# Optimization experiments

Measured on AMD Instinct MI355X. Metric: run time of the kernel, lower is better.

The kernel has to match this reference:

```python
import jax, jax.numpy as jnp
import numpy as np

S, T, H, D = 4096, 4096, 16, 64
N_EMBD = H * D

def setup_inputs() -> dict:
    key = jax.random.key(0)
    kq, kk, kv, kw = jax.random.split(key, 4)
    q = jax.random.normal(kq, (S, H, D), dtype=jnp.float32)
    k = jax.random.normal(kk, (T, H, D), dtype=jnp.float32)
    v = jax.random.normal(kv, (T, H, D), dtype=jnp.float32)
    # GPT-2 style init: std = 0.02 / sqrt(2 * n_layer), n_layer = 24
    W_proj = jax.random.normal(kw, (N_EMBD, N_EMBD), dtype=jnp.float32) * (0.02 / np.sqrt(2 * 24))
    return {"q": q, "k": k, "v": v, "W_proj": W_proj}

def reference(q, k, v, W_proj):
    s, h, d = q.shape
    t = k.shape[0]
    # causal bias: mask positions where query index < key index (future keys)
    causal_bias = (jnp.arange(s)[:, None] < jnp.arange(t)[None, :]).astype(jnp.float32) * -10000.0
    scale = 1.0 / jnp.sqrt(jnp.float32(d))
    # [h, s, t] scores in fp32 (matches original .astype(jnp.float32))
    scores = jnp.einsum('shd,thd->hst', q, k).astype(jnp.float32) * scale + causal_bias
    attn = jax.nn.softmax(scores, axis=-1).astype(q.dtype)
    # dropout p=0 / inference -> identity
    out = jnp.einsum('hst,thd->shd', attn, v).reshape(s, h * d)
    # nn.Linear (no bias) vmapped over tokens: y = x @ W.T
    return out @ W_proj.T
```

## Files before the change

kernel.cpp:

```cpp
#include <hip/hip_runtime.h>

#define S_LEN 4096
#define NH 16
#define DH 64
#define NE 1024

typedef __bf16 bf16_t;
typedef __bf16 bf16x8 __attribute__((ext_vector_type(8)));
typedef __bf16 bf16x4 __attribute__((ext_vector_type(4)));
typedef __bf16 bf16x2 __attribute__((ext_vector_type(2)));
typedef float  f32x4  __attribute__((ext_vector_type(4)));

#define QSCALE 0.180336879f

__global__ __launch_bounds__(256) void pack_all(const float* __restrict__ q,
                                                const float* __restrict__ k,
                                                const float* __restrict__ w,
                                                const float* __restrict__ v,
                                                bf16_t* __restrict__ qb,
                                                bf16_t* __restrict__ kb,
                                                bf16_t* __restrict__ wb,
                                                bf16_t* __restrict__ vt) {
    __shared__ bf16_t tile[64][65];
    const int bid = blockIdx.x;
    if (bid < 4096) {
        const int tid = bid * 256 + threadIdx.x;
        const int e = tid * 4;
        const int s = e >> 10;
        const int c = e & (NE - 1);
        const int h = c >> 6;
        const int d = c & (DH - 1);
        const int o = (h * S_LEN + s) * DH + d;
        float4 qv = *(const float4*)(q + e);
        float4 kv = *(const float4*)(k + e);
        bf16x4 qo, ko;
        qo[0] = (bf16_t)(qv.x * QSCALE); qo[1] = (bf16_t)(qv.y * QSCALE);
        qo[2] = (bf16_t)(qv.z * QSCALE); qo[3] = (bf16_t)(qv.w * QSCALE);
        ko[0] = (bf16_t)kv.x; ko[1] = (bf16_t)kv.y; ko[2] = (bf16_t)kv.z; ko[3] = (bf16_t)kv.w;
        *(bf16x4*)(qb + o) = qo;
        *(bf16x4*)(kb + o) = ko;
        if (tid < (NE * NE / 4)) {
            float4 wv = *(const float4*)(w + tid * 4);
            bf16x4 wo;
            wo[0] = (bf16_t)wv.x; wo[1] = (bf16_t)wv.y; wo[2] = (bf16_t)wv.z; wo[3] = (bf16_t)wv.w;
            *(bf16x4*)(wb + tid * 4) = wo;
        }
    } else {
        const int vb = bid - 4096;
        const int h  = vb >> 6;
        const int t0 = (vb & 63) * 64;
        const int r  = threadIdx.x >> 6;
        const int cl = threadIdx.x & 63;
#pragma unroll
        for (int rep = 0; rep < 16; ++rep) {
            int i = rep * 4 + r;
            tile[cl][i] = (bf16_t)v[(t0 + i) * NE + h * DH + cl];
        }
        __syncthreads();
        const int r2  = threadIdx.x >> 5;
        const int cl2 = (threadIdx.x & 31) * 2;
#pragma unroll
        for (int rep = 0; rep < 8; ++rep) {
            int d = rep * 8 + r2;
            bf16x2 out;
            out[0] = tile[d][cl2];
            out[1] = tile[d][cl2 + 1];
            *(bf16x2*)(vt + (h * DH + d) * S_LEN + t0 + cl2) = out;
        }
    }
}

__global__ __launch_bounds__(512, 4) void attn(const bf16_t* __restrict__ qb,
                                               const bf16_t* __restrict__ kb,
                                               const bf16_t* __restrict__ vt,
                                               float* __restrict__ po,
                                               float* __restrict__ ls) {
    __shared__ __align__(16) bf16_t kbuf[2][64 * 72];
    __shared__ __align__(16) bf16_t vbuf[2][64 * 72];
    __shared__ __align__(16) bf16_t pbuf[8][16 * 72];

    const int tid  = threadIdx.x;
    const int wave = tid >> 6;
    const int lane = tid & 63;
    const int l15  = lane & 15;
    const int quad = lane >> 4;
    const int h = blockIdx.x;
    const int x = blockIdx.y;

    const int sA = x;
    const int sB = 31 - x;
    const int n0 = x + 1;
    const int b1 = sB + 1;
    const int N  = 33;

    const bf16_t* __restrict__ qh = qb + h * (S_LEN * DH);
    const bf16_t* __restrict__ kh = kb + h * (S_LEN * DH);
    const bf16_t* __restrict__ vh = vt + h * (DH * S_LEN);

    const int row0 = tid >> 3;
    const int tc8  = (tid & 7) * 8;

    f32x4 o_acc[4];
    float lsum[4];
    bf16x8 qA[2];
    int s0 = sA * 128 + wave * 16;

    auto load_q = [&](int s0_) {
#pragma unroll
        for (int dc = 0; dc < 2; ++dc)
            qA[dc] = *(const bf16x8*)(qh + (s0_ + l15) * DH + dc * 32 + quad * 8);
    };
    auto reset_acc = [&]() {
#pragma unroll
        for (int db = 0; db < 4; ++db) o_acc[db] = (f32x4){0.f, 0.f, 0.f, 0.f};
#pragma unroll
        for (int r = 0; r < 4; ++r) lsum[r] = 0.0f;
    };
    auto epilogue = [&](int s0_, int slot) {
        float l2[4];
#pragma unroll
        for (int r = 0; r < 4; ++r) l2[r] = lsum[r];
#pragma unroll
        for (int off = 8; off >= 1; off >>= 1)
#pragma unroll
            for (int r = 0; r < 4; ++r) l2[r] += __shfl_xor(l2[r], off, 64);
        float* poz = po + (size_t)(slot * NH + h) * S_LEN * DH;
#pragma unroll
        for (int db = 0; db < 4; ++db)
#pragma unroll
            for (int r = 0; r < 4; ++r)
                poz[(s0_ + quad * 4 + r) * DH + db * 16 + l15] = o_acc[db][r];
        if (l15 == 0) {
            float* lsz = ls + (size_t)(slot * NH + h) * S_LEN;
#pragma unroll
            for (int r = 0; r < 4; ++r) lsz[s0_ + quad * 4 + r] = l2[r];
        }
    };

    load_q(s0);
    reset_acc();

    {
        bf16x8 kr = *(const bf16x8*)(kh + row0 * DH + tc8);
        bf16x8 vr = *(const bf16x8*)(vh + row0 * S_LEN + tc8);
        *(bf16x8*)(kbuf[0] + row0 * 72 + tc8) = kr;
        *(bf16x8*)(vbuf[0] + row0 * 72 + tc8) = vr;
    }
    __syncthreads();

    for (int j = 0; j < N; ++j) {
        if (j == n0) {
            epilogue(s0, 0);
            s0 = sB * 128 + wave * 16;
            load_q(s0);
            reset_acc();
        }
        const int t0 = (j < n0 ? j : b1 + (j - n0)) * 64;
        const bf16_t* kb_ = kbuf[j & 1];
        const bf16_t* vb_ = vbuf[j & 1];

        bf16x8 krn, vrn;
        const bool pf = (j + 1 < N);
        if (pf) {
            const int jn = j + 1;
            const int tn = (jn < n0 ? jn : b1 + (jn - n0)) * 64;
            krn = *(const bf16x8*)(kh + (tn + row0) * DH + tc8);
            vrn = *(const bf16x8*)(vh + row0 * S_LEN + tn + tc8);
        }

        f32x4 c_[4];
#pragma unroll
        for (int ch = 0; ch < 4; ++ch) {
            bf16x8 kB0 = *(const bf16x8*)(kb_ + (ch * 16 + l15) * 72 + quad * 8);
            bf16x8 kB1 = *(const bf16x8*)(kb_ + (ch * 16 + l15) * 72 + 32 + quad * 8);
            f32x4 zr = (f32x4){0.f, 0.f, 0.f, 0.f};
            zr = __builtin_amdgcn_mfma_f32_16x16x32_bf16(qA[0], kB0, zr, 0, 0, 0);
            zr = __builtin_amdgcn_mfma_f32_16x16x32_bf16(qA[1], kB1, zr, 0, 0, 0);
            c_[ch] = zr;
        }

        if (t0 + 63 > s0) {
#pragma unroll
            for (int ch = 0; ch < 4; ++ch) {
                int col = t0 + ch * 16 + l15;
#pragma unroll
                for (int r = 0; r < 4; ++r) {
                    int row = s0 + quad * 4 + r;
                    if (col > row) c_[ch][r] = -INFINITY;
                }
            }
        }

        bf16_t* pl = pbuf[wave];
#pragma unroll
        for (int ch = 0; ch < 4; ++ch)
#pragma unroll
            for (int r = 0; r < 4; ++r) {
                float p = exp2f(c_[ch][r] - 17.0f);
                lsum[r] += p;
                pl[(quad * 4 + r) * 72 + ch * 16 + l15] = (bf16_t)p;
            }

        __builtin_amdgcn_wave_barrier();

        bf16x8 pA[2];
#pragma unroll
        for (int kc = 0; kc < 2; ++kc)
            pA[kc] = *(const bf16x8*)(pbuf[wave] + l15 * 72 + kc * 32 + quad * 8);

        bf16x8 vB[4][2];
#pragma unroll
        for (int db = 0; db < 4; ++db)
#pragma unroll
            for (int kc = 0; kc < 2; ++kc)
                vB[db][kc] = *(const bf16x8*)(vb_ + (db * 16 + l15) * 72 + kc * 32 + quad * 8);

#pragma unroll
        for (int db = 0; db < 4; ++db) {
            o_acc[db] = __builtin_amdgcn_mfma_f32_16x16x32_bf16(pA[0], vB[db][0], o_acc[db], 0, 0, 0);
            o_acc[db] = __builtin_amdgcn_mfma_f32_16x16x32_bf16(pA[1], vB[db][1], o_acc[db], 0, 0, 0);
        }

        if (pf) {
            *(bf16x8*)(kbuf[(j + 1) & 1] + row0 * 72 + tc8) = krn;
            *(bf16x8*)(vbuf[(j + 1) & 1] + row0 * 72 + tc8) = vrn;
        }
        __syncthreads();
    }

    epilogue(s0, 1);
}

__global__ __launch_bounds__(256) void combine(const float* __restrict__ po,
                                               const float* __restrict__ ls,
                                               bf16_t* __restrict__ xb) {
    const int idx = blockIdx.x * 256 + threadIdx.x;
    const int row = idx >> 8;
    const int c   = (idx & 255) * 4;
    const int h   = c >> 6;
    const int d   = c & 63;
    const size_t base0 = (size_t)(h) * S_LEN * DH + row * DH + d;
    const size_t base1 = (size_t)(NH + h) * S_LEN * DH + row * DH + d;
    float4 o0 = *(const float4*)(po + base0);
    float4 o1 = *(const float4*)(po + base1);
    float l = ls[(size_t)h * S_LEN + row] + ls[(size_t)(NH + h) * S_LEN + row];
    float inv = 1.0f / l;
    bf16x4 out;
    out[0] = (bf16_t)((o0.x + o1.x) * inv);
    out[1] = (bf16_t)((o0.y + o1.y) * inv);
    out[2] = (bf16_t)((o0.z + o1.z) * inv);
    out[3] = (bf16_t)((o0.w + o1.w) * inv);
    *(bf16x4*)(xb + (size_t)row * NE + c) = out;
}

__global__ __launch_bounds__(256, 4) void proj(const bf16_t* __restrict__ xb,
                                               const bf16_t* __restrict__ wb,
                                               float* __restrict__ y) {
    __shared__ __align__(16) bf16_t wbuf[2][64 * 72];
    const int tid  = threadIdx.x;
    const int wave = tid >> 6;
    const int lane = tid & 63;
    const int l15  = lane & 15;
    const int quad = lane >> 4;
    const int m0 = blockIdx.x * 64 + wave * 16;
    const int n0 = blockIdx.y * 64;

    const int row0 = tid >> 3;
    const int tc8  = (tid & 7) * 8;

    f32x4 acc[4];
#pragma unroll
    for (int nb = 0; nb < 4; ++nb) acc[nb] = (f32x4){0.f, 0.f, 0.f, 0.f};

    {
        bf16x8 wr0 = *(const bf16x8*)(wb + (n0 + row0) * NE + tc8);
        bf16x8 wr1 = *(const bf16x8*)(wb + (n0 + row0 + 32) * NE + tc8);
        *(bf16x8*)(wbuf[0] + row0 * 72 + tc8) = wr0;
        *(bf16x8*)(wbuf[0] + (row0 + 32) * 72 + tc8) = wr1;
    }
    bf16x8 a[2];
#pragma unroll
    for (int kc = 0; kc < 2; ++kc)
        a[kc] = *(const bf16x8*)(xb + (m0 + l15) * NE + kc * 32 + quad * 8);
    __syncthreads();

    for (int kt = 0; kt < 16; ++kt) {
        const bf16_t* wb_ = wbuf[kt & 1];
        const bool pf = (kt + 1 < 16);
        bf16x8 wr0, wr1, an[2];
        if (pf) {
            const int kn = (kt + 1) * 64;
            wr0 = *(const bf16x8*)(wb + (n0 + row0) * NE + kn + tc8);
            wr1 = *(const bf16x8*)(wb + (n0 + row0 + 32) * NE + kn + tc8);
#pragma unroll
            for (int kc = 0; kc < 2; ++kc)
                an[kc] = *(const bf16x8*)(xb + (m0 + l15) * NE + kn + kc * 32 + quad * 8);
        }

#pragma unroll
        for (int nb = 0; nb < 4; ++nb)
#pragma unroll
            for (int kc = 0; kc < 2; ++kc) {
                bf16x8 b = *(const bf16x8*)(wb_ + (nb * 16 + l15) * 72 + kc * 32 + quad * 8);
                acc[nb] = __builtin_amdgcn_mfma_f32_16x16x32_bf16(a[kc], b, acc[nb], 0, 0, 0);
            }

        if (pf) {
            *(bf16x8*)(wbuf[(kt + 1) & 1] + row0 * 72 + tc8) = wr0;
            *(bf16x8*)(wbuf[(kt + 1) & 1] + (row0 + 32) * 72 + tc8) = wr1;
#pragma unroll
            for (int kc = 0; kc < 2; ++kc) a[kc] = an[kc];
        }
        __syncthreads();
    }

#pragma unroll
    for (int nb = 0; nb < 4; ++nb)
#pragma unroll
        for (int r = 0; r < 4; ++r)
            y[(m0 + quad * 4 + r) * NE + n0 + nb * 16 + l15] = acc[nb][r];
}

extern "C" void kernel_launch(void* const* d_in, const int* in_sizes, int n_in,
                              void* d_out, int out_size, void* d_ws, size_t ws_size,
                              hipStream_t stream) {
    const float* q = (const float*)d_in[0];
    const float* k = (const float*)d_in[1];
    const float* v = (const float*)d_in[2];
    const float* w = (const float*)d_in[3];
    float* y = (float*)d_out;

    bf16_t* ws = (bf16_t*)d_ws;
    bf16_t* qb = ws;
    bf16_t* kb = qb + 4 * 1024 * 1024;
    bf16_t* vt = kb + 4 * 1024 * 1024;
    bf16_t* wb = vt + 4 * 1024 * 1024;
    bf16_t* xb = wb + 1024 * 1024;
    float*  po = (float*)(xb + 4 * 1024 * 1024);
    float*  ls = po + (size_t)2 * NH * S_LEN * DH;

    pack_all<<<dim3(4096 + 1024), dim3(256), 0, stream>>>(q, k, w, v, qb, kb, wb, vt);
    attn<<<dim3(NH, 32), dim3(512), 0, stream>>>(qb, kb, vt, po, ls);
    combine<<<dim3(4096), dim3(256), 0, stream>>>(po, ls, xb);
    proj<<<dim3(S_LEN / 64, NE / 64), dim3(256), 0, stream>>>(xb, wb, y);
}
```

Before: 197.6 us.

## Give each attention wave 32 query rows and halve block size to 256

Each wave now handles two 16-row query groups instead of one, so every K/V fragment read from shared memory feeds twice as many MFMAs. The block shrinks from 8 to 4 waves, and each thread now loads two rows of K and V per tile. The P staging buffer gains an XOR swizzle to cut LDS bank conflicts. The trade-off is more registers per wave and fewer waves per CU to hide latency.

```diff
diff --git a/kernel.cpp b/kernel.cpp
--- a/kernel.cpp
+++ b/kernel.cpp
@@ -70,14 +70,14 @@
     }
 }
 
-__global__ __launch_bounds__(512, 4) void attn(const bf16_t* __restrict__ qb,
+__global__ __launch_bounds__(256, 2) void attn(const bf16_t* __restrict__ qb,
                                                const bf16_t* __restrict__ kb,
                                                const bf16_t* __restrict__ vt,
                                                float* __restrict__ po,
                                                float* __restrict__ ls) {
     __shared__ __align__(16) bf16_t kbuf[2][64 * 72];
     __shared__ __align__(16) bf16_t vbuf[2][64 * 72];
-    __shared__ __align__(16) bf16_t pbuf[8][16 * 72];
+    __shared__ __align__(16) bf16_t pbuf[4][32 * 72];
 
     const int tid  = threadIdx.x;
     const int wave = tid >> 6;
@@ -100,40 +100,53 @@
     const int row0 = tid >> 3;
     const int tc8  = (tid & 7) * 8;
 
-    f32x4 o_acc[4];
-    float lsum[4];
-    bf16x8 qA[2];
-    int s0 = sA * 128 + wave * 16;
+    f32x4 o_acc[2][4];
+    float lsum[2][4];
+    bf16x8 qA[2][2];
+    int s0 = sA * 128 + wave * 32;
 
     auto load_q = [&](int s0_) {
 #pragma unroll
-        for (int dc = 0; dc < 2; ++dc)
-            qA[dc] = *(const bf16x8*)(qh + (s0_ + l15) * DH + dc * 32 + quad * 8);
+        for (int g = 0; g < 2; ++g)
+#pragma unroll
+            for (int dc = 0; dc < 2; ++dc)
+                qA[g][dc] = *(const bf16x8*)(qh + (s0_ + g * 16 + l15) * DH + dc * 32 + quad * 8);
     };
     auto reset_acc = [&]() {
 #pragma unroll
-        for (int db = 0; db < 4; ++db) o_acc[db] = (f32x4){0.f, 0.f, 0.f, 0.f};
-#pragma unroll
-        for (int r = 0; r < 4; ++r) lsum[r] = 0.0f;
+        for (int g = 0; g < 2; ++g) {
+#pragma unroll
+            for (int db = 0; db < 4; ++db) o_acc[g][db] = (f32x4){0.f, 0.f, 0.f, 0.f};
+#pragma unroll
+            for (int r = 0; r < 4; ++r) lsum[g][r] = 0.0f;
+        }
     };
     auto epilogue = [&](int s0_, int slot) {
-        float l2[4];
-#pragma unroll
-        for (int r = 0; r < 4; ++r) l2[r] = lsum[r];
+        float l2[2][4];
+#pragma unroll
+        for (int g = 0; g < 2; ++g)
+#pragma unroll
+            for (int r = 0; r < 4; ++r) l2[g][r] = lsum[g][r];
 #pragma unroll
         for (int off = 8; off >= 1; off >>= 1)
 #pragma unroll
-            for (int r = 0; r < 4; ++r) l2[r] += __shfl_xor(l2[r], off, 64);
+            for (int g = 0; g < 2; ++g)
+#pragma unroll
+                for (int r = 0; r < 4; ++r) l2[g][r] += __shfl_xor(l2[g][r], off, 64);
         float* poz = po + (size_t)(slot * NH + h) * S_LEN * DH;
 #pragma unroll
-        for (int db = 0; db < 4; ++db)
-#pragma unroll
-            for (int r = 0; r < 4; ++r)
-                poz[(s0_ + quad * 4 + r) * DH + db * 16 + l15] = o_acc[db][r];
+        for (int g = 0; g < 2; ++g)
+#pragma unroll
+            for (int db = 0; db < 4; ++db)
+#pragma unroll
+                for (int r = 0; r < 4; ++r)
+                    poz[(s0_ + g * 16 + quad * 4 + r) * DH + db * 16 + l15] = o_acc[g][db][r];
         if (l15 == 0) {
             float* lsz = ls + (size_t)(slot * NH + h) * S_LEN;
 #pragma unroll
-            for (int r = 0; r < 4; ++r) lsz[s0_ + quad * 4 + r] = l2[r];
+            for (int g = 0; g < 2; ++g)
+#pragma unroll
+                for (int r = 0; r < 4; ++r) lsz[s0_ + g * 16 + quad * 4 + r] = l2[g][r];
         }
     };
 
@@ -141,17 +154,21 @@
     reset_acc();
 
     {
-        bf16x8 kr = *(const bf16x8*)(kh + row0 * DH + tc8);
-        bf16x8 vr = *(const bf16x8*)(vh + row0 * S_LEN + tc8);
-        *(bf16x8*)(kbuf[0] + row0 * 72 + tc8) = kr;
-        *(bf16x8*)(vbuf[0] + row0 * 72 + tc8) = vr;
+        bf16x8 kr0 = *(const bf16x8*)(kh + row0 * DH + tc8);
+        bf16x8 kr1 = *(const bf16x8*)(kh + (row0 + 32) * DH + tc8);
+        bf16x8 vr0 = *(const bf16x8*)(vh + row0 * S_LEN + tc8);
+        bf16x8 vr1 = *(const bf16x8*)(vh + (row0 + 32) * S_LEN + tc8);
+        *(bf16x8*)(kbuf[0] + row0 * 72 + tc8) = kr0;
+        *(bf16x8*)(kbuf[0] + (row0 + 32) * 72 + tc8) = kr1;
+        *(bf16x8*)(vbuf[0] + row0 * 72 + tc8) = vr0;
+        *(bf16x8*)(vbuf[0] + (row0 + 32) * 72 + tc8) = vr1;
     }
     __syncthreads();
 
     for (int j = 0; j < N; ++j) {
         if (j == n0) {
             epilogue(s0, 0);
-            s0 = sB * 128 + wave * 16;
+            s0 = sB * 128 + wave * 32;
             load_q(s0);
             reset_acc();
         }
@@ -159,54 +176,69 @@
         const bf16_t* kb_ = kbuf[j & 1];
         const bf16_t* vb_ = vbuf[j & 1];
 
-        bf16x8 krn, vrn;
+        bf16x8 kr0n, kr1n, vr0n, vr1n;
         const bool pf = (j + 1 < N);
         if (pf) {
             const int jn = j + 1;
             const int tn = (jn < n0 ? jn : b1 + (jn - n0)) * 64;
-            krn = *(const bf16x8*)(kh + (tn + row0) * DH + tc8);
-            vrn = *(const bf16x8*)(vh + row0 * S_LEN + tn + tc8);
-        }
-
-        f32x4 c_[4];
+            kr0n = *(const bf16x8*)(kh + (tn + row0) * DH + tc8);
+            kr1n = *(const bf16x8*)(kh + (tn + row0 + 32) * DH + tc8);
+            vr0n = *(const bf16x8*)(vh + row0 * S_LEN + tn + tc8);
+            vr1n = *(const bf16x8*)(vh + (row0 + 32) * S_LEN + tn + tc8);
+        }
+
+        f32x4 c_[2][4];
 #pragma unroll
         for (int ch = 0; ch < 4; ++ch) {
             bf16x8 kB0 = *(const bf16x8*)(kb_ + (ch * 16 + l15) * 72 + quad * 8);
             bf16x8 kB1 = *(const bf16x8*)(kb_ + (ch * 16 + l15) * 72 + 32 + quad * 8);
-            f32x4 zr = (f32x4){0.f, 0.f, 0.f, 0.f};
-            zr = __builtin_amdgcn_mfma_f32_16x16x32_bf16(qA[0], kB0, zr, 0, 0, 0);
-            zr = __builtin_amdgcn_mfma_f32_16x16x32_bf16(qA[1], kB1, zr, 0, 0, 0);
-            c_[ch] = zr;
+#pragma unroll
+            for (int g = 0; g < 2; ++g) {
+                f32x4 zr = (f32x4){0.f, 0.f, 0.f, 0.f};
+                zr = __builtin_amdgcn_mfma_f32_16x16x32_bf16(qA[g][0], kB0, zr, 0, 0, 0);
+                zr = __builtin_amdgcn_mfma_f32_16x16x32_bf16(qA[g][1], kB1, zr, 0, 0, 0);
+                c_[g][ch] = zr;
+            }
         }
 
         if (t0 + 63 > s0) {
 #pragma unroll
-            for (int ch = 0; ch < 4; ++ch) {
-                int col = t0 + ch * 16 + l15;
+            for (int g = 0; g < 2; ++g)
+#pragma unroll
+                for (int ch = 0; ch < 4; ++ch) {
+                    int col = t0 + ch * 16 + l15;
+#pragma unroll
+                    for (int r = 0; r < 4; ++r) {
+                        int row = s0 + g * 16 + quad * 4 + r;
+                        if (col > row) c_[g][ch][r] = -INFINITY;
+                    }
+                }
+        }
+
+        bf16_t* pl = pbuf[wave];
+#pragma unroll
+        for (int g = 0; g < 2; ++g) {
+            const int pswz = ((g * 4 + quad) & 7) * 8;
+#pragma unroll
+            for (int ch = 0; ch < 4; ++ch)
 #pragma unroll
                 for (int r = 0; r < 4; ++r) {
-                    int row = s0 + quad * 4 + r;
-                    if (col > row) c_[ch][r] = -INFINITY;
+                    float p = exp2f(c_[g][ch][r] - 17.0f);
+                    lsum[g][r] += p;
+                    pl[(g * 16 + quad * 4 + r) * 72 + ((ch * 16 + l15) ^ pswz)] = (bf16_t)p;
                 }
-            }
-        }
-
-        bf16_t* pl = pbuf[wave];
-#pragma unroll
-        for (int ch = 0; ch < 4; ++ch)
-#pragma unroll
-            for (int r = 0; r < 4; ++r) {
-                float p = exp2f(c_[ch][r] - 17.0f);
-                lsum[r] += p;
-                pl[(quad * 4 + r) * 72 + ch * 16 + l15] = (bf16_t)p;
-            }
+        }
 
         __builtin_amdgcn_wave_barrier();
 
-        bf16x8 pA[2];
-#pragma unroll
-        for (int kc = 0; kc < 2; ++kc)
-            pA[kc] = *(const bf16x8*)(pbuf[wave] + l15 * 72 + kc * 32 + quad * 8);
+        bf16x8 pA[2][2];
+#pragma unroll
+        for (int g = 0; g < 2; ++g) {
+            const int rswz = ((g * 4 + (l15 >> 2)) & 7) * 8;
+#pragma unroll
+            for (int kc = 0; kc < 2; ++kc)
+                pA[g][kc] = *(const bf16x8*)(pl + (g * 16 + l15) * 72 + ((kc * 32 + quad * 8) ^ rswz));
+        }
 
         bf16x8 vB[4][2];
 #pragma unroll
@@ -216,14 +248,20 @@
                 vB[db][kc] = *(const bf16x8*)(vb_ + (db * 16 + l15) * 72 + kc * 32 + quad * 8);
 
 #pragma unroll
-        for (int db = 0; db < 4; ++db) {
-            o_acc[db] = __builtin_amdgcn_mfma_f32_16x16x32_bf16(pA[0], vB[db][0], o_acc[db], 0, 0, 0);
-            o_acc[db] = __builtin_amdgcn_mfma_f32_16x16x32_bf16(pA[1], vB[db][1], o_acc[db], 0, 0, 0);
-        }
+        for (int g = 0; g < 2; ++g)
+#pragma unroll
+            for (int db = 0; db < 4; ++db) {
+                o_acc[g][db] = __builtin_amdgcn_mfma_f32_16x16x32_bf16(pA[g][0], vB[db][0], o_acc[g][db], 0, 0, 0);
+                o_acc[g][db] = __builtin_amdgcn_mfma_f32_16x16x32_bf16(pA[g][1], vB[db][1], o_acc[g][db], 0, 0, 0);
+            }
 
         if (pf) {
-            *(bf16x8*)(kbuf[(j + 1) & 1] + row0 * 72 + tc8) = krn;
-            *(bf16x8*)(vbuf[(j + 1) & 1] + row0 * 72 + tc8) = vrn;
+            bf16_t* kd = kbuf[(j + 1) & 1];
+            bf16_t* vd = vbuf[(j + 1) & 1];
+            *(bf16x8*)(kd + row0 * 72 + tc8) = kr0n;
+            *(bf16x8*)(kd + (row0 + 32) * 72 + tc8) = kr1n;
+            *(bf16x8*)(vd + row0 * 72 + tc8) = vr0n;
+            *(bf16x8*)(vd + (row0 + 32) * 72 + tc8) = vr1n;
         }
         __syncthreads();
     }
@@ -340,7 +378,7 @@
     float*  ls = po + (size_t)2 * NH * S_LEN * DH;
 
     pack_all<<<dim3(4096 + 1024), dim3(256), 0, stream>>>(q, k, w, v, qb, kb, wb, vt);
-    attn<<<dim3(NH, 32), dim3(512), 0, stream>>>(qb, kb, vt, po, ls);
+    attn<<<dim3(NH, 32), dim3(256), 0, stream>>>(qb, kb, vt, po, ls);
     combine<<<dim3(4096), dim3(256), 0, stream>>>(po, ls, xb);
     proj<<<dim3(S_LEN / 64, NE / 64), dim3(256), 0, stream>>>(xb, wb, y);
 }
```

Measured after the change: 200.9 us. Within noise of the previous version (+1.7%).

## Compute transposed scores to keep P in registers, skip fully masked tiles

Applied to the files above, without the earlier changes.

Swaps the MFMA operands so each lane holds scores for one query across several keys. The exp'd probabilities can then be packed straight into the A operand of the PV MFMA, with no round trip through a per-wave LDS buffer and no wave barrier. The V operand loads are regathered as two bf16x4 halves to match the new key ordering. The kernel also skips compute for wave tiles and 16-key chunks that lie entirely above the causal diagonal, and simplifies the row-sum reduction to two shuffles.

```diff
diff --git a/kernel.cpp b/kernel.cpp
--- a/kernel.cpp
+++ b/kernel.cpp
@@ -77,7 +77,6 @@
                                                float* __restrict__ ls) {
     __shared__ __align__(16) bf16_t kbuf[2][64 * 72];
     __shared__ __align__(16) bf16_t vbuf[2][64 * 72];
-    __shared__ __align__(16) bf16_t pbuf[8][16 * 72];
 
     const int tid  = threadIdx.x;
     const int wave = tid >> 6;
@@ -101,7 +100,7 @@
     const int tc8  = (tid & 7) * 8;
 
     f32x4 o_acc[4];
-    float lsum[4];
+    float lsum;
     bf16x8 qA[2];
     int s0 = sA * 128 + wave * 16;
 
@@ -113,27 +112,21 @@
     auto reset_acc = [&]() {
 #pragma unroll
         for (int db = 0; db < 4; ++db) o_acc[db] = (f32x4){0.f, 0.f, 0.f, 0.f};
-#pragma unroll
-        for (int r = 0; r < 4; ++r) lsum[r] = 0.0f;
+        lsum = 0.0f;
     };
     auto epilogue = [&](int s0_, int slot) {
-        float l2[4];
-#pragma unroll
-        for (int r = 0; r < 4; ++r) l2[r] = lsum[r];
-#pragma unroll
-        for (int off = 8; off >= 1; off >>= 1)
-#pragma unroll
-            for (int r = 0; r < 4; ++r) l2[r] += __shfl_xor(l2[r], off, 64);
+        float l2 = lsum;
+        l2 += __shfl_xor(l2, 16, 64);
+        l2 += __shfl_xor(l2, 32, 64);
         float* poz = po + (size_t)(slot * NH + h) * S_LEN * DH;
 #pragma unroll
         for (int db = 0; db < 4; ++db)
 #pragma unroll
             for (int r = 0; r < 4; ++r)
                 poz[(s0_ + quad * 4 + r) * DH + db * 16 + l15] = o_acc[db][r];
-        if (l15 == 0) {
+        if (lane < 16) {
             float* lsz = ls + (size_t)(slot * NH + h) * S_LEN;
-#pragma unroll
-            for (int r = 0; r < 4; ++r) lsz[s0_ + quad * 4 + r] = l2[r];
+            lsz[s0_ + lane] = l2;
         }
     };
 
@@ -168,57 +161,63 @@
             vrn = *(const bf16x8*)(vh + row0 * S_LEN + tn + tc8);
         }
 
-        f32x4 c_[4];
-#pragma unroll
-        for (int ch = 0; ch < 4; ++ch) {
-            bf16x8 kB0 = *(const bf16x8*)(kb_ + (ch * 16 + l15) * 72 + quad * 8);
-            bf16x8 kB1 = *(const bf16x8*)(kb_ + (ch * 16 + l15) * 72 + 32 + quad * 8);
-            f32x4 zr = (f32x4){0.f, 0.f, 0.f, 0.f};
-            zr = __builtin_amdgcn_mfma_f32_16x16x32_bf16(qA[0], kB0, zr, 0, 0, 0);
-            zr = __builtin_amdgcn_mfma_f32_16x16x32_bf16(qA[1], kB1, zr, 0, 0, 0);
-            c_[ch] = zr;
-        }
-
-        if (t0 + 63 > s0) {
+        if (t0 <= s0 + 15) {
+            f32x4 c_[4];
 #pragma unroll
             for (int ch = 0; ch < 4; ++ch) {
-                int col = t0 + ch * 16 + l15;
-#pragma unroll
-                for (int r = 0; r < 4; ++r) {
-                    int row = s0 + quad * 4 + r;
-                    if (col > row) c_[ch][r] = -INFINITY;
+                bf16x8 kB0 = *(const bf16x8*)(kb_ + (ch * 16 + l15) * 72 + quad * 8);
+                bf16x8 kB1 = *(const bf16x8*)(kb_ + (ch * 16 + l15) * 72 + 32 + quad * 8);
+                f32x4 zr = (f32x4){0.f, 0.f, 0.f, 0.f};
+                zr = __builtin_amdgcn_mfma_f32_16x16x32_bf16(kB0, qA[0], zr, 0, 0, 0);
+                zr = __builtin_amdgcn_mfma_f32_16x16x32_bf16(kB1, qA[1], zr, 0, 0, 0);
+                c_[ch] = zr;
+            }
+
+            const int query = s0 + l15;
+            float p[4][4];
+#pragma unroll
+            for (int ch = 0; ch < 4; ++ch) {
+                if (t0 + ch * 16 <= s0 + 15) {
+                    const bool edge = (t0 + ch * 16 + 15 > s0);
+#pragma unroll
+                    for (int r = 0; r < 4; ++r) {
+                        float cc = c_[ch][r];
+                        if (edge) {
+                            int key = t0 + ch * 16 + quad * 4 + r;
+                            if (key > query) cc = -INFINITY;
+                        }
+                        float pv = exp2f(cc - 17.0f);
+                        lsum += pv;
+                        p[ch][r] = pv;
+                    }
+                } else {
+#pragma unroll
+                    for (int r = 0; r < 4; ++r) p[ch][r] = 0.0f;
                 }
             }
-        }
-
-        bf16_t* pl = pbuf[wave];
-#pragma unroll
-        for (int ch = 0; ch < 4; ++ch)
-#pragma unroll
-            for (int r = 0; r < 4; ++r) {
-                float p = exp2f(c_[ch][r] - 17.0f);
-                lsum[r] += p;
-                pl[(quad * 4 + r) * 72 + ch * 16 + l15] = (bf16_t)p;
-            }
-
-        __builtin_amdgcn_wave_barrier();
-
-        bf16x8 pA[2];
-#pragma unroll
-        for (int kc = 0; kc < 2; ++kc)
-            pA[kc] = *(const bf16x8*)(pbuf[wave] + l15 * 72 + kc * 32 + quad * 8);
-
-        bf16x8 vB[4][2];
-#pragma unroll
-        for (int db = 0; db < 4; ++db)
-#pragma unroll
-            for (int kc = 0; kc < 2; ++kc)
-                vB[db][kc] = *(const bf16x8*)(vb_ + (db * 16 + l15) * 72 + kc * 32 + quad * 8);
-
-#pragma unroll
-        for (int db = 0; db < 4; ++db) {
-            o_acc[db] = __builtin_amdgcn_mfma_f32_16x16x32_bf16(pA[0], vB[db][0], o_acc[db], 0, 0, 0);
-            o_acc[db] = __builtin_amdgcn_mfma_f32_16x16x32_bf16(pA[1], vB[db][1], o_acc[db], 0, 0, 0);
+
+            bf16x8 pA[2];
+#pragma unroll
+            for (int kc = 0; kc < 2; ++kc) {
+                bf16x8 t;
+                t[0] = (bf16_t)p[2 * kc][0];     t[1] = (bf16_t)p[2 * kc][1];
+                t[2] = (bf16_t)p[2 * kc][2];     t[3] = (bf16_t)p[2 * kc][3];
+                t[4] = (bf16_t)p[2 * kc + 1][0]; t[5] = (bf16_t)p[2 * kc + 1][1];
+                t[6] = (bf16_t)p[2 * kc + 1][2]; t[7] = (bf16_t)p[2 * kc + 1][3];
+                pA[kc] = t;
+            }
+
+#pragma unroll
+            for (int db = 0; db < 4; ++db) {
+#pragma unroll
+                for (int kc = 0; kc < 2; ++kc) {
+                    const bf16_t* vrow = vb_ + (db * 16 + l15) * 72 + kc * 32 + quad * 4;
+                    bf16x4 lo = *(const bf16x4*)(vrow);
+                    bf16x4 hi = *(const bf16x4*)(vrow + 16);
+                    bf16x8 vB = __builtin_shufflevector(lo, hi, 0, 1, 2, 3, 4, 5, 6, 7);
+                    o_acc[db] = __builtin_amdgcn_mfma_f32_16x16x32_bf16(pA[kc], vB, o_acc[db], 0, 0, 0);
+                }
+            }
         }
 
         if (pf) {
```

Measured after the change: 207.3 us. 4.9% more time.
